# Kernel optimization log

Measured on AMD Instinct MI355X. Metric: run time of the kernel, lower is better.

## Reference

```python
import jax, jax.numpy as jnp
import numpy as np

B, S, H, NH, HD = 64, 200, 1024, 16, 64
MAX_LEN = 200
FF = 4 * H


def _ln(x, g, b):
    m = x.mean(-1, keepdims=True)
    v = ((x - m) ** 2).mean(-1, keepdims=True)
    return (x - m) / jnp.sqrt(v + 1e-5) * g + b


def setup_inputs() -> dict:
    key = jax.random.key(0)
    k = jax.random.split(key, 24)
    s = 0.02
    f32 = jnp.float32
    return {
        "x": jax.random.normal(k[0], (B, S, H), f32),
        "time": jax.random.uniform(k[1], (B, S, 1), dtype=f32),
        "wq": jax.random.normal(k[2], (H, H), f32) * s,
        "bq": jnp.zeros((H,), f32),
        "wk": jax.random.normal(k[3], (H, H), f32) * s,
        "bk": jnp.zeros((H,), f32),
        "wv": jax.random.normal(k[4], (H, H), f32) * s,
        "bv": jnp.zeros((H,), f32),
        "wo": jax.random.normal(k[5], (H, H), f32) * s,
        "bo": jnp.zeros((H,), f32),
        "wt": jax.random.normal(k[6], (1, H), f32) * s,
        "bt": jnp.zeros((H,), f32),
        "pos_embed": jax.random.normal(k[7], (2 * MAX_LEN - 1, HD), f32) * s,
        "g1": jnp.ones((H,), f32),
        "be1": jnp.zeros((H,), f32),
        "g2": jnp.ones((H,), f32),
        "be2": jnp.zeros((H,), f32),
        "w1": jax.random.normal(k[8], (H, FF), f32) * s,
        "bf1": jnp.zeros((FF,), f32),
        "w2": jax.random.normal(k[9], (FF, H), f32) * s,
        "bf2": jnp.zeros((H,), f32),
    }


def reference(x, time, wq, bq, wk, bk, wv, bv, wo, bo, wt, bt, pos_embed,
              g1, be1, g2, be2, w1, bf1, w2, bf2):
    b, s, hs = x.shape
    residual = x
    h = _ln(x, g1, be1)
    h = h + time @ wt + bt  # time embedding added post-LN
    q = (h @ wq + bq).reshape(b, s, NH, HD).transpose(0, 2, 1, 3)  # [b,h,s,d]
    k = (h @ wk + bk).reshape(b, s, NH, HD).transpose(0, 2, 1, 3)
    v = (h @ wv + bv).reshape(b, s, NH, HD).transpose(0, 2, 1, 3)
    scale = np.float32(1.0 / np.sqrt(HD))
    scores = jnp.einsum('bhqd,bhkd->bhqk', q, k) * scale
    # gathered relative position bias (NOT scaled, added after scaling)
    idx = jnp.arange(s)
    rel = jnp.clip(idx[:, None] - idx[None, :] + (MAX_LEN - 1), 0, 2 * MAX_LEN - 2)
    rel_emb = pos_embed[rel]  # [s, s, HD]
    scores = scores + jnp.einsum('bhqd,qkd->bhqk', q, rel_emb)
    causal_mask = jnp.triu(jnp.ones((s, s), bool), 1)
    scores = jnp.where(causal_mask, jnp.float32(-1e9), scores)
    attn = jax.nn.softmax(scores, axis=-1)
    ctx = jnp.einsum('bhqk,bhkd->bhqd', attn, v)
    ctx = ctx.transpose(0, 2, 1, 3).reshape(b, s, hs)
    out = ctx @ wo + bo + residual
    res2 = out
    h2 = _ln(out, g2, be2)
    ff = jax.nn.gelu(h2 @ w1 + bf1, approximate=False) @ w2 + bf2
    return ff + res2
```

## Files before the change

kernel.cpp:

```cpp
#include <hip/hip_runtime.h>

#define B_SZ   64
#define S_LEN  200
#define H_DIM  1024
#define NHEAD  16
#define HDIM   64
#define FF_DIM 4096
#define NROWS  (B_SZ * S_LEN)

typedef __bf16 bf16x8 __attribute__((ext_vector_type(8)));
typedef float  f32x4  __attribute__((ext_vector_type(4)));

#define GLOBAL_AS __attribute__((address_space(1)))
#define LDS_AS    __attribute__((address_space(3)))

__device__ __forceinline__ void g2lds16(const void* g, void* l) {
  __builtin_amdgcn_global_load_lds((const GLOBAL_AS void*)g, (LDS_AS void*)l, 16, 0, 0);
}

__device__ __forceinline__ float b2f(ushort u) {
  return __uint_as_float(((unsigned int)u) << 16);
}
__device__ __forceinline__ ushort f2b(float f) {
  unsigned int u = __float_as_uint(f);
  u += 0x7fffu + ((u >> 16) & 1u);
  return (ushort)(u >> 16);
}
__device__ __forceinline__ bf16x8 ld_g16(const ushort* p) {
  union { uint4 u; bf16x8 v; } r; r.u = *(const uint4*)p; return r.v;
}
__device__ __forceinline__ bf16x8 ld_lds8x2(const ushort* p) {
  union { uint2 u[2]; bf16x8 v; } r;
  r.u[0] = *(const uint2*)p;
  r.u[1] = *(const uint2*)(p + 4);
  return r.v;
}

__global__ __launch_bounds__(256) void transpose_to_bf16(
    const float* __restrict__ w, ushort* __restrict__ wt, int K, int N) {
  __shared__ float tile[32][33];
  int nb = blockIdx.x * 32, kb = blockIdx.y * 32;
  int tx = threadIdx.x, ty = threadIdx.y;
#pragma unroll
  for (int i = 0; i < 4; ++i) {
    int k = kb + ty + i * 8;
    tile[ty + i * 8][tx] = w[(size_t)k * N + nb + tx];
  }
  __syncthreads();
#pragma unroll
  for (int i = 0; i < 4; ++i) {
    int n = nb + ty + i * 8;
    wt[(size_t)n * K + kb + tx] = f2b(tile[tx][ty + i * 8]);
  }
}

__global__ void concat_bias(const float* __restrict__ bq, const float* __restrict__ bk,
                            const float* __restrict__ bv, float* __restrict__ o) {
  int i = blockIdx.x * 256 + threadIdx.x;
  if (i < 1024) o[i] = bq[i];
  else if (i < 2048) o[i] = bk[i - 1024];
  else if (i < 3072) o[i] = bv[i - 2048];
}

__global__ void pos_to_bf16(const float* __restrict__ pos, ushort* __restrict__ pb) {
  int i = blockIdx.x * 256 + threadIdx.x;
  pb[i] = f2b(pos[(size_t)199 * 64 + i]);
}

template <int HAS_TIME>
__global__ __launch_bounds__(256) void ln_kernel(
    const float* __restrict__ x, const float* __restrict__ g, const float* __restrict__ be,
    const float* __restrict__ tv, const float* __restrict__ wt, const float* __restrict__ bt,
    ushort* __restrict__ out) {
  int r = blockIdx.x, t = threadIdx.x;
  const float4* xr = (const float4*)(x + (size_t)r * H_DIM);
  float4 xv = xr[t];
  float s  = xv.x + xv.y + xv.z + xv.w;
  float s2 = xv.x * xv.x + xv.y * xv.y + xv.z * xv.z + xv.w * xv.w;
#pragma unroll
  for (int off = 32; off; off >>= 1) {
    s  += __shfl_xor(s, off);
    s2 += __shfl_xor(s2, off);
  }
  __shared__ float red[8];
  int lane = t & 63, wid = t >> 6;
  if (lane == 0) { red[wid] = s; red[4 + wid] = s2; }
  __syncthreads();
  float S  = red[0] + red[1] + red[2] + red[3];
  float S2 = red[4] + red[5] + red[6] + red[7];
  float m    = S * (1.0f / H_DIM);
  float var  = S2 * (1.0f / H_DIM) - m * m;
  float rstd = rsqrtf(var + 1e-5f);
  float tval = HAS_TIME ? tv[r] : 0.0f;
  float4 gv = ((const float4*)g)[t];
  float4 bv = ((const float4*)be)[t];
  float v0 = (xv.x - m) * rstd * gv.x + bv.x;
  float v1 = (xv.y - m) * rstd * gv.y + bv.y;
  float v2 = (xv.z - m) * rstd * gv.z + bv.z;
  float v3 = (xv.w - m) * rstd * gv.w + bv.w;
  if (HAS_TIME) {
    float4 wv = ((const float4*)wt)[t];
    float4 btv = ((const float4*)bt)[t];
    v0 += tval * wv.x + btv.x;
    v1 += tval * wv.y + btv.y;
    v2 += tval * wv.z + btv.z;
    v3 += tval * wv.w + btv.w;
  }
  ushort4 o;
  o.x = f2b(v0); o.y = f2b(v1); o.z = f2b(v2); o.w = f2b(v3);
  ((ushort4*)(out + (size_t)r * H_DIM))[t] = o;
}

template <int EPI>
__global__ __launch_bounds__(256) void gemm_bt(
    const ushort* __restrict__ A, const ushort* __restrict__ Bt,
    const float* __restrict__ bias, void* __restrict__ Cv,
    const float* __restrict__ resid, int M, int N, int K) {
  __shared__ __align__(16) ushort As[2 * 128 * 32];
  __shared__ __align__(16) ushort Bs[2 * 128 * 32];
  int t = threadIdx.x;
  int lane = t & 63, wave = t >> 6;
  int wm = wave >> 1, wn = wave & 1;
  int r15 = lane & 15, quad = lane >> 4;
  int nwg = gridDim.x * gridDim.y;
  int bid = blockIdx.y * gridDim.x + blockIdx.x;
  int swz = (bid & 7) * (nwg >> 3) + (bid >> 3);
  int bx = swz % gridDim.x, by = swz / gridDim.x;
  size_t row0 = (size_t)by * 128;
  size_t col0 = (size_t)bx * 128;

  int srow = (lane >> 2), scol = (lane & 3) * 8;
  const ushort* ga0 = A  + (row0 + wave * 32 +      srow) * K + scol;
  const ushort* ga1 = A  + (row0 + wave * 32 + 16 + srow) * K + scol;
  const ushort* gb0 = Bt + (col0 + wave * 32 +      srow) * K + scol;
  const ushort* gb1 = Bt + (col0 + wave * 32 + 16 + srow) * K + scol;
  ushort* la0 = As + (wave * 32) * 32;
  ushort* la1 = As + (wave * 32 + 16) * 32;
  ushort* lb0 = Bs + (wave * 32) * 32;
  ushort* lb1 = Bs + (wave * 32 + 16) * 32;

  f32x4 acc[4][4] = {};

  for (int k0 = 0; k0 < K; k0 += 64) {
#pragma unroll
    for (int kh = 0; kh < 2; ++kh) {
      int go = k0 + kh * 32, lo = kh * 4096;
      g2lds16(ga0 + go, la0 + lo);
      g2lds16(ga1 + go, la1 + lo);
      g2lds16(gb0 + go, lb0 + lo);
      g2lds16(gb1 + go, lb1 + lo);
    }
    __syncthreads();
#pragma unroll
    for (int kh = 0; kh < 2; ++kh) {
      bf16x8 af[4], bfr[4];
#pragma unroll
      for (int i = 0; i < 4; ++i)
        af[i] = *(const bf16x8*)&As[kh * 4096 + (wm * 64 + i * 16 + r15) * 32 + quad * 8];
#pragma unroll
      for (int j = 0; j < 4; ++j)
        bfr[j] = *(const bf16x8*)&Bs[kh * 4096 + (wn * 64 + j * 16 + r15) * 32 + quad * 8];
#pragma unroll
      for (int i = 0; i < 4; ++i)
#pragma unroll
        for (int j = 0; j < 4; ++j)
          acc[i][j] = __builtin_amdgcn_mfma_f32_16x16x32_bf16(af[i], bfr[j], acc[i][j], 0, 0, 0);
    }
    __syncthreads();
  }

  int mbase = (int)row0 + wm * 64;
  int nbase = (int)col0 + wn * 64;
#pragma unroll
  for (int i = 0; i < 4; ++i) {
#pragma unroll
    for (int j = 0; j < 4; ++j) {
      int col = nbase + j * 16 + r15;
      float bb = bias[col];
#pragma unroll
      for (int ii = 0; ii < 4; ++ii) {
        int row = mbase + i * 16 + quad * 4 + ii;
        size_t idx = (size_t)row * N + col;
        float v = acc[i][j][ii] + bb;
        if constexpr (EPI == 0) {
          ((ushort*)Cv)[idx] = f2b(v);
        } else if constexpr (EPI == 1) {
          float gl = 0.5f * v * (1.0f + erff(v * 0.70710678118f));
          ((ushort*)Cv)[idx] = f2b(gl);
        } else {
          ((float*)Cv)[idx] = v + resid[idx];
        }
      }
    }
  }
}

template <int IB>
__device__ __forceinline__ void mfma_blk(f32x4 (&acc)[8][4],
                                         const bf16x8 (&af)[4], const bf16x8 (&bfr)[4]) {
#pragma unroll
  for (int i = 0; i < 4; ++i)
#pragma unroll
    for (int j = 0; j < 4; ++j)
      acc[IB + i][j] =
          __builtin_amdgcn_mfma_f32_16x16x32_bf16(af[i], bfr[j], acc[IB + i][j], 0, 0, 0);
}

__device__ __forceinline__ bf16x8 rdfrag(const ushort* plane, int r, int quad) {
  return *(const bf16x8*)(plane + r * 32 + ((quad ^ ((r >> 1) & 3)) << 3));
}

__device__ __forceinline__ void read_q0(bf16x8 (&af)[4], bf16x8 (&bfr)[4],
                                        const ushort* pA, const ushort* pB,
                                        int wn1, int r15, int quad) {
#pragma unroll
  for (int j = 0; j < 4; ++j) bfr[j] = rdfrag(pB, wn1 * 64 + j * 16 + r15, quad);
#pragma unroll
  for (int i = 0; i < 4; ++i) af[i] = rdfrag(pA, i * 16 + r15, quad);
}
__device__ __forceinline__ void read_q1(bf16x8 (&af)[4], const ushort* pA,
                                        int r15, int quad) {
#pragma unroll
  for (int i = 0; i < 4; ++i) af[i] = rdfrag(pA, 64 + i * 16 + r15, quad);
}

#define VMW8() asm volatile("s_waitcnt vmcnt(8)" ::: "memory")
#define VMW4() asm volatile("s_waitcnt vmcnt(4)" ::: "memory")
#define VMW0() asm volatile("s_waitcnt vmcnt(0)" ::: "memory")
#define BARX() __builtin_amdgcn_s_barrier()
#define PRIO1() __builtin_amdgcn_s_setprio(1)
#define PRIO0() __builtin_amdgcn_s_setprio(0)

template <int EPI>
__global__ __launch_bounds__(512) void gemm256(
    const ushort* __restrict__ A, const ushort* __restrict__ Bt,
    const float* __restrict__ bias, void* __restrict__ Cv,
    const float* __restrict__ resid, int M, int N, int K) {
  __shared__ __align__(16) ushort lds[2][2][2][2][4096];
  const int t = threadIdx.x;
  const int lane = t & 63, wave = t >> 6;
  const int wm = wave >> 2;
  const int wn = wave & 3;
  const int wn1 = wn & 1;
  const int bh = wn >> 1;
  const int r15 = lane & 15, quad = lane >> 4;
  int nwg = gridDim.x * gridDim.y;
  int bid = blockIdx.y * gridDim.x + blockIdx.x;
  int swz = (bid & 7) * (nwg >> 3) + (bid >> 3);
  int bx = swz % gridDim.x, by = swz / gridDim.x;
  const size_t row0 = (size_t)by * 256;
  const size_t col0 = (size_t)bx * 256;

  const int gwA = wave & 3;
  const int gwB = ((wave >> 1) & 2) | (wave & 1);

  const ushort *gA0, *gA1, *gB0, *gB1;
  {
    int p0 = gwA * 128 + lane;
    int p1 = p0 + 64;
    int ra0 = p0 >> 2, sa0 = (p0 & 3) ^ ((p0 >> 3) & 3);
    int ra1 = p1 >> 2, sa1 = (p1 & 3) ^ ((p1 >> 3) & 3);
    gA0 = A + (row0 + wm * 128 + ra0) * K + sa0 * 8;
    gA1 = A + (row0 + wm * 128 + ra1) * K + sa1 * 8;
    int q0 = gwB * 128 + lane;
    int q1 = q0 + 64;
    int rb0 = q0 >> 2, sb0 = (q0 & 3) ^ ((q0 >> 3) & 3);
    int rb1 = q1 >> 2, sb1 = (q1 & 3) ^ ((q1 >> 3) & 3);
    gB0 = Bt + (col0 + bh * 128 + rb0) * K + sb0 * 8;
    gB1 = Bt + (col0 + bh * 128 + rb1) * K + sb1 * 8;
  }
  const int ldsA0 = gwA * 1024, ldsA1 = gwA * 1024 + 512;
  const int ldsB0 = gwB * 1024, ldsB1 = gwB * 1024 + 512;

#define STAGE_A(nb_, skh_, kof_)                                        \
  do {                                                                  \
    g2lds16(gA0 + (kof_) + (skh_) * 32, &lds[nb_][0][wm][skh_][ldsA0]); \
    g2lds16(gA1 + (kof_) + (skh_) * 32, &lds[nb_][0][wm][skh_][ldsA1]); \
  } while (0)
#define STAGE_B(nb_, skh_, kof_)                                        \
  do {                                                                  \
    g2lds16(gB0 + (kof_) + (skh_) * 32, &lds[nb_][1][bh][skh_][ldsB0]); \
    g2lds16(gB1 + (kof_) + (skh_) * 32, &lds[nb_][1][bh][skh_][ldsB1]); \
  } while (0)
#define PAP(b_, k_) (&lds[b_][0][wm][k_][0])
#define PBP(b_, k_) (&lds[b_][1][bh][k_][0])

  f32x4 acc[8][4] = {};

  STAGE_A(0, 0, 0);
  STAGE_B(0, 0, 0);
  STAGE_A(0, 1, 0);
  STAGE_B(0, 1, 0);
  STAGE_A(1, 0, 64);
  STAGE_B(1, 0, 64);
  VMW8();
  BARX();

#define ITER_BODY(LAST_, ka_)                                                  \
  {                                                                            \
    bf16x8 af[4], bfr[4];                                                      \
                                                          \
    read_q0(af, bfr, PAP(0, 0), PBP(0, 0), wn1, r15, quad);                    \
    STAGE_A(1, 1, (ka_) + 64);                                                 \
    BARX(); PRIO1(); mfma_blk<0>(acc, af, bfr); PRIO0(); BARX();               \
                                                          \
    read_q1(af, PAP(0, 0), r15, quad);                                         \
    STAGE_B(1, 1, (ka_) + 64);                                                 \
    BARX(); PRIO1(); mfma_blk<4>(acc, af, bfr); PRIO0();                       \
    VMW8(); BARX();                                                            \
                                                          \
    read_q0(af, bfr, PAP(0, 1), PBP(0, 1), wn1, r15, quad);                    \
    if (!(LAST_)) STAGE_A(0, 0, (ka_) + 128);                                  \
    BARX(); PRIO1(); mfma_blk<0>(acc, af, bfr); PRIO0(); BARX();               \
                                                          \
    read_q1(af, PAP(0, 1), r15, quad);                                         \
    if (!(LAST_)) STAGE_B(0, 0, (ka_) + 128);                                  \
    BARX(); PRIO1(); mfma_blk<4>(acc, af, bfr); PRIO0();                       \
    if (LAST_) { VMW4(); } else { VMW8(); }                                    \
    BARX();                                                                    \
                                                          \
    read_q0(af, bfr, PAP(1, 0), PBP(1, 0), wn1, r15, quad);                    \
    if (!(LAST_)) STAGE_A(0, 1, (ka_) + 128);                                  \
    BARX(); PRIO1(); mfma_blk<0>(acc, af, bfr); PRIO0(); BARX();               \
                                                          \
    read_q1(af, PAP(1, 0), r15, quad);                                         \
    if (!(LAST_)) STAGE_B(0, 1, (ka_) + 128);                                  \
    BARX(); PRIO1(); mfma_blk<4>(acc, af, bfr); PRIO0();                       \
    if (LAST_) { VMW0(); } else { VMW8(); }                                    \
    BARX();                                                                    \
                                                          \
    read_q0(af, bfr, PAP(1, 1), PBP(1, 1), wn1, r15, quad);                    \
    if (!(LAST_)) STAGE_A(1, 0, (ka_) + 192);                                  \
    BARX(); PRIO1(); mfma_blk<0>(acc, af, bfr); PRIO0(); BARX();               \
                                                          \
    read_q1(af, PAP(1, 1), r15, quad);                                         \
    if (!(LAST_)) STAGE_B(1, 0, (ka_) + 192);                                  \
    BARX(); PRIO1(); mfma_blk<4>(acc, af, bfr); PRIO0();                       \
    if (!(LAST_)) { VMW8(); }                                                  \
    BARX();                                                                    \
  }

  const int NI = K >> 7;
  for (int it = 0; it < NI - 1; ++it) {
    ITER_BODY(0, it << 7);
  }
  ITER_BODY(1, (NI - 1) << 7);
#undef ITER_BODY

  int mbase = (int)row0 + wm * 128;
  int nbase = (int)col0 + wn * 64;
#pragma unroll
  for (int j = 0; j < 4; ++j) {
    int col = nbase + j * 16 + r15;
    float bb = bias[col];
#pragma unroll
    for (int i = 0; i < 8; ++i) {
#pragma unroll
      for (int ii = 0; ii < 4; ++ii) {
        int row = mbase + i * 16 + quad * 4 + ii;
        size_t idx = (size_t)row * N + col;
        float v = acc[i][j][ii] + bb;
        if constexpr (EPI == 0) {
          ((ushort*)Cv)[idx] = f2b(v);
        } else if constexpr (EPI == 1) {
          float gl = 0.5f * v * (1.0f + erff(v * 0.70710678118f));
          ((ushort*)Cv)[idx] = f2b(gl);
        } else {
          ((float*)Cv)[idx] = v + resid[idx];
        }
      }
    }
  }
#undef STAGE_A
#undef STAGE_B
#undef PAP
#undef PBP
}

#define PW_STRIDE 228
__global__ __launch_bounds__(256) void attn_kernel(
    const ushort* __restrict__ qkv, const ushort* __restrict__ pos_bf,
    ushort* __restrict__ ctx) {
  int bh = blockIdx.x;
  int b = bh >> 4, h = bh & 15;
  __shared__ ushort Vt[64][PW_STRIDE];
  __shared__ ushort Pw[4][16][PW_STRIDE];
  int t = threadIdx.x, lane = t & 63, wave = t >> 6;
  int r15 = lane & 15, quad = lane >> 4;
  const size_t base = ((size_t)b * S_LEN) * 3072 + (size_t)h * 64;

  for (int i = t; i < 64 * 28; i += 256) Vt[i / 28][200 + (i % 28)] = 0;
  for (int i = t; i < 800; i += 256) {
    int kp = i >> 3, d0 = (i & 7) * 8;
    int k = kp * 2;
    union { uint4 v; ushort u[8]; } r0, r1;
    r0.v = *(const uint4*)&qkv[base + (size_t)k * 3072 + 2048 + d0];
    r1.v = *(const uint4*)&qkv[base + (size_t)(k + 1) * 3072 + 2048 + d0];
#pragma unroll
    for (int j = 0; j < 8; ++j) {
      ushort2 w2; w2.x = r0.u[j]; w2.y = r1.u[j];
      *(ushort2*)&Vt[d0 + j][k] = w2;
    }
  }
  __syncthreads();

  for (int qt = wave; qt < 13; qt += 4) {
    int q0 = qt * 16;
    int qrow = q0 + r15; if (qrow > 199) qrow = 199;
    const ushort* qp = qkv + base + (size_t)qrow * 3072;
    bf16x8 aq0 = ld_g16(qp + quad * 8);
    bf16x8 aq1 = ld_g16(qp + 32 + quad * 8);
    ushort* pw = &Pw[wave][0][0];

#pragma unroll
    for (int dt = 0; dt < 13; ++dt) {
      if (dt > qt) continue;
      int prow = dt * 16 + r15; if (prow > 199) prow = 199;
      const ushort* pp = pos_bf + (size_t)prow * 64;
      bf16x8 p0 = ld_g16(pp + quad * 8);
      bf16x8 p1 = ld_g16(pp + 32 + quad * 8);
      f32x4 tt = {};
      tt = __builtin_amdgcn_mfma_f32_16x16x32_bf16(aq0, p0, tt, 0, 0, 0);
      tt = __builtin_amdgcn_mfma_f32_16x16x32_bf16(aq1, p1, tt, 0, 0, 0);
#pragma unroll
      for (int ii = 0; ii < 4; ++ii)
        pw[(quad * 4 + ii) * PW_STRIDE + dt * 16 + r15] = f2b(tt[ii]);
    }

    f32x4 sreg[13];
    float rowmax[4] = {-3.0e38f, -3.0e38f, -3.0e38f, -3.0e38f};
#pragma unroll
    for (int kt = 0; kt < 13; ++kt) {
      if (kt > qt) continue;
      int krow = kt * 16 + r15; if (krow > 199) krow = 199;
      const ushort* kp = qkv + base + (size_t)krow * 3072 + 1024;
      bf16x8 k0 = ld_g16(kp + quad * 8);
      bf16x8 k1 = ld_g16(kp + 32 + quad * 8);
      f32x4 s = {};
      s = __builtin_amdgcn_mfma_f32_16x16x32_bf16(aq0, k0, s, 0, 0, 0);
      s = __builtin_amdgcn_mfma_f32_16x16x32_bf16(aq1, k1, s, 0, 0, 0);
      int k = kt * 16 + r15;
#pragma unroll
      for (int ii = 0; ii < 4; ++ii) {
        int q = q0 + quad * 4 + ii;
        float v;
        if (k <= q) {
          v = s[ii] * 0.125f + b2f(pw[(quad * 4 + ii) * PW_STRIDE + (q - k)]);
        } else {
          v = -1.0e30f;
        }
        s[ii] = v;
        rowmax[ii] = fmaxf(rowmax[ii], v);
      }
      sreg[kt] = s;
    }
#pragma unroll
    for (int off = 8; off; off >>= 1)
#pragma unroll
      for (int ii = 0; ii < 4; ++ii)
        rowmax[ii] = fmaxf(rowmax[ii], __shfl_xor(rowmax[ii], off));

    float rsum[4] = {0.f, 0.f, 0.f, 0.f};
#pragma unroll
    for (int kt = 0; kt < 13; ++kt) {
      if (kt > qt) continue;
#pragma unroll
      for (int ii = 0; ii < 4; ++ii) {
        float e = __expf(sreg[kt][ii] - rowmax[ii]);
        rsum[ii] += e;
        pw[(quad * 4 + ii) * PW_STRIDE + kt * 16 + r15] = f2b(e);
      }
    }
    if ((qt & 1) == 0) {
#pragma unroll
      for (int ii = 0; ii < 4; ++ii)
        pw[(quad * 4 + ii) * PW_STRIDE + (qt + 1) * 16 + r15] = 0;
    }
#pragma unroll
    for (int off = 8; off; off >>= 1)
#pragma unroll
      for (int ii = 0; ii < 4; ++ii)
        rsum[ii] += __shfl_xor(rsum[ii], off);
    float rinv[4];
#pragma unroll
    for (int ii = 0; ii < 4; ++ii) rinv[ii] = 1.0f / rsum[ii];

    int nk = (q0 + 15) / 32 + 1;
    f32x4 acc[4] = {};
#pragma unroll
    for (int k32 = 0; k32 < 7; ++k32) {
      if (k32 >= nk) continue;
      bf16x8 ap = ld_lds8x2(&pw[r15 * PW_STRIDE + k32 * 32 + quad * 8]);
#pragma unroll
      for (int n = 0; n < 4; ++n) {
        bf16x8 bv = ld_lds8x2(&Vt[n * 16 + r15][k32 * 32 + quad * 8]);
        acc[n] = __builtin_amdgcn_mfma_f32_16x16x32_bf16(ap, bv, acc[n], 0, 0, 0);
      }
    }
#pragma unroll
    for (int n = 0; n < 4; ++n)
#pragma unroll
      for (int ii = 0; ii < 4; ++ii) {
        int q = q0 + quad * 4 + ii;
        if (q < S_LEN)
          ctx[((size_t)(b * S_LEN + q)) * H_DIM + h * 64 + n * 16 + r15] =
              f2b(acc[n][ii] * rinv[ii]);
      }
  }
}

extern "C" void kernel_launch(void* const* d_in, const int* in_sizes, int n_in,
                              void* d_out, int out_size, void* d_ws, size_t ws_size,
                              hipStream_t stream) {
  (void)in_sizes; (void)n_in; (void)out_size; (void)ws_size;
  const float* x    = (const float*)d_in[0];
  const float* timev= (const float*)d_in[1];
  const float* wq   = (const float*)d_in[2];
  const float* bq   = (const float*)d_in[3];
  const float* wk   = (const float*)d_in[4];
  const float* bk   = (const float*)d_in[5];
  const float* wv   = (const float*)d_in[6];
  const float* bv   = (const float*)d_in[7];
  const float* wo   = (const float*)d_in[8];
  const float* bo   = (const float*)d_in[9];
  const float* wt   = (const float*)d_in[10];
  const float* bt   = (const float*)d_in[11];
  const float* pos  = (const float*)d_in[12];
  const float* g1   = (const float*)d_in[13];
  const float* be1  = (const float*)d_in[14];
  const float* g2   = (const float*)d_in[15];
  const float* be2  = (const float*)d_in[16];
  const float* w1   = (const float*)d_in[17];
  const float* bf1  = (const float*)d_in[18];
  const float* w2   = (const float*)d_in[19];
  const float* bf2  = (const float*)d_in[20];

  char* ws = (char*)d_ws;
  ushort* wqkv_t = (ushort*)ws;   ws += (size_t)3072 * 1024 * 2;
  ushort* wo_t   = (ushort*)ws;   ws += (size_t)1024 * 1024 * 2;
  ushort* w1_t   = (ushort*)ws;   ws += (size_t)4096 * 1024 * 2;
  ushort* w2_t   = (ushort*)ws;   ws += (size_t)1024 * 4096 * 2;
  float*  bqkv   = (float*)ws;    ws += (size_t)16384;
  ushort* pos_bf = (ushort*)ws;   ws += (size_t)200 * 64 * 2;
  char* r1 = ws;                  ws += (size_t)NROWS * 3072 * 2;
  ushort* qkv  = (ushort*)r1;
  ushort* h2   = (ushort*)r1;
  ushort* gbuf = (ushort*)(r1 + (size_t)NROWS * H_DIM * 2);
  char* r2 = ws;                  ws += (size_t)NROWS * 1024 * 2;
  ushort* hbf = (ushort*)r2;
  ushort* ctx = (ushort*)r2;
  float* res2 = (float*)d_out;

  dim3 tb(32, 8);
  transpose_to_bf16<<<dim3(32, 32), tb, 0, stream>>>(wq, wqkv_t,                 1024, 1024);
  transpose_to_bf16<<<dim3(32, 32), tb, 0, stream>>>(wk, wqkv_t + 1024 * 1024,   1024, 1024);
  transpose_to_bf16<<<dim3(32, 32), tb, 0, stream>>>(wv, wqkv_t + 2048 * 1024,   1024, 1024);
  transpose_to_bf16<<<dim3(32, 32), tb, 0, stream>>>(wo, wo_t,                   1024, 1024);
  transpose_to_bf16<<<dim3(128, 32), tb, 0, stream>>>(w1, w1_t,                  1024, 4096);
  transpose_to_bf16<<<dim3(32, 128), tb, 0, stream>>>(w2, w2_t,                  4096, 1024);
  concat_bias<<<12, 256, 0, stream>>>(bq, bk, bv, bqkv);
  pos_to_bf16<<<50, 256, 0, stream>>>(pos, pos_bf);

  ln_kernel<1><<<NROWS, 256, 0, stream>>>(x, g1, be1, timev, wt, bt, hbf);

  gemm256<0><<<dim3(12, 50), 512, 0, stream>>>(hbf, wqkv_t, bqkv, qkv, nullptr,
                                               NROWS, 3072, 1024);
  attn_kernel<<<B_SZ * NHEAD, 256, 0, stream>>>(qkv, pos_bf, ctx);

  gemm256<2><<<dim3(4, 50), 512, 0, stream>>>(ctx, wo_t, bo, res2, x,
                                              NROWS, 1024, 1024);
  ln_kernel<0><<<NROWS, 256, 0, stream>>>(res2, g2, be2, nullptr, nullptr, nullptr, h2);

  for (int c = 0; c < 2; ++c) {
    size_t ro = (size_t)c * 6400;
    gemm256<1><<<dim3(16, 25), 512, 0, stream>>>(h2 + ro * 1024, w1_t, bf1, gbuf, nullptr,
                                                 6400, 4096, 1024);
    gemm_bt<2><<<dim3(8, 50), 256, 0, stream>>>(gbuf, w2_t, bf2, (float*)d_out + ro * 1024,
                                                res2 + ro * 1024, 6400, 1024, 4096);
  }
}
```

Measured before the change: 802.0 us.

## Merge prep kernels, use wave-per-row LayerNorm, reorder tile swizzle and attention tiles

Replaces the eight weight-transpose, bias-concat and pos-conversion launches with a single prep kernel. LayerNorm now handles one row per wave, which removes the LDS reduction and block barrier. GEMM tile swizzle now maps consecutive swizzled ids along M rather than N. GEMM epilogues hoist the bias loads and iterate rows before columns. Attention waves take query tiles in a permuted order to balance causal work. Together these cut launch overhead and sync cost but change cache reuse patterns for the GEMMs.

```diff
diff --git a/kernel.cpp b/kernel.cpp
--- a/kernel.cpp
+++ b/kernel.cpp
@@ -36,35 +36,47 @@
   return r.v;
 }
 
-__global__ __launch_bounds__(256) void transpose_to_bf16(
-    const float* __restrict__ w, ushort* __restrict__ wt, int K, int N) {
-  __shared__ float tile[32][33];
-  int nb = blockIdx.x * 32, kb = blockIdx.y * 32;
-  int tx = threadIdx.x, ty = threadIdx.y;
-#pragma unroll
-  for (int i = 0; i < 4; ++i) {
-    int k = kb + ty + i * 8;
-    tile[ty + i * 8][tx] = w[(size_t)k * N + nb + tx];
-  }
-  __syncthreads();
-#pragma unroll
-  for (int i = 0; i < 4; ++i) {
-    int n = nb + ty + i * 8;
-    wt[(size_t)n * K + kb + tx] = f2b(tile[tx][ty + i * 8]);
-  }
-}
-
-__global__ void concat_bias(const float* __restrict__ bq, const float* __restrict__ bk,
-                            const float* __restrict__ bv, float* __restrict__ o) {
-  int i = blockIdx.x * 256 + threadIdx.x;
-  if (i < 1024) o[i] = bq[i];
-  else if (i < 2048) o[i] = bk[i - 1024];
-  else if (i < 3072) o[i] = bv[i - 2048];
-}
-
-__global__ void pos_to_bf16(const float* __restrict__ pos, ushort* __restrict__ pb) {
-  int i = blockIdx.x * 256 + threadIdx.x;
-  pb[i] = f2b(pos[(size_t)199 * 64 + i]);
+__global__ __launch_bounds__(256) void prep_kernel(
+    const float* __restrict__ wq, const float* __restrict__ wk,
+    const float* __restrict__ wv, const float* __restrict__ wo,
+    const float* __restrict__ w1, const float* __restrict__ w2,
+    const float* __restrict__ bq, const float* __restrict__ bk,
+    const float* __restrict__ bv_, const float* __restrict__ pos,
+    ushort* __restrict__ wqkv_t, ushort* __restrict__ wo_t,
+    ushort* __restrict__ w1_t, ushort* __restrict__ w2_t,
+    float* __restrict__ bqkv, ushort* __restrict__ pos_bf) {
+  int id = blockIdx.x;
+  if (id < 12288) {
+    const float* src; ushort* dst; int K, N, tile;
+    if (id < 4096) {
+      K = 1024; N = 1024; tile = id & 1023;
+      int m = id >> 10;
+      src = (m == 0) ? wq : (m == 1) ? wk : (m == 2) ? wv : wo;
+      dst = (m == 3) ? wo_t : wqkv_t + (size_t)m * 1024 * 1024;
+    } else if (id < 8192) {
+      K = 1024; N = 4096; tile = id - 4096; src = w1; dst = w1_t;
+    } else {
+      K = 4096; N = 1024; tile = id - 8192; src = w2; dst = w2_t;
+    }
+    int nx = N >> 5;
+    int nb = (tile % nx) * 32, kb = (tile / nx) * 32;
+    __shared__ float t32[32][33];
+    int tx = threadIdx.x & 31, ty = threadIdx.x >> 5;
+#pragma unroll
+    for (int i = 0; i < 4; ++i)
+      t32[ty + i * 8][tx] = src[(size_t)(kb + ty + i * 8) * N + nb + tx];
+    __syncthreads();
+#pragma unroll
+    for (int i = 0; i < 4; ++i)
+      dst[(size_t)(nb + ty + i * 8) * K + kb + tx] = f2b(t32[tx][ty + i * 8]);
+  } else {
+    int t = threadIdx.x;
+    for (int i = t; i < 1024; i += 256) {
+      bqkv[i] = bq[i]; bqkv[1024 + i] = bk[i]; bqkv[2048 + i] = bv_[i];
+    }
+    for (int i = t; i < 12800; i += 256)
+      pos_bf[i] = f2b(pos[(size_t)199 * 64 + i]);
+  }
 }
 
 template <int HAS_TIME>
@@ -72,43 +84,47 @@
     const float* __restrict__ x, const float* __restrict__ g, const float* __restrict__ be,
     const float* __restrict__ tv, const float* __restrict__ wt, const float* __restrict__ bt,
     ushort* __restrict__ out) {
-  int r = blockIdx.x, t = threadIdx.x;
+  int wave = threadIdx.x >> 6, lane = threadIdx.x & 63;
+  int r = blockIdx.x * 4 + wave;
   const float4* xr = (const float4*)(x + (size_t)r * H_DIM);
-  float4 xv = xr[t];
-  float s  = xv.x + xv.y + xv.z + xv.w;
-  float s2 = xv.x * xv.x + xv.y * xv.y + xv.z * xv.z + xv.w * xv.w;
+  float4 xv[4];
+  float s = 0.f, s2 = 0.f;
+#pragma unroll
+  for (int k = 0; k < 4; ++k) {
+    xv[k] = xr[lane + 64 * k];
+    s  += xv[k].x + xv[k].y + xv[k].z + xv[k].w;
+    s2 += xv[k].x * xv[k].x + xv[k].y * xv[k].y + xv[k].z * xv[k].z + xv[k].w * xv[k].w;
+  }
 #pragma unroll
   for (int off = 32; off; off >>= 1) {
     s  += __shfl_xor(s, off);
     s2 += __shfl_xor(s2, off);
   }
-  __shared__ float red[8];
-  int lane = t & 63, wid = t >> 6;
-  if (lane == 0) { red[wid] = s; red[4 + wid] = s2; }
-  __syncthreads();
-  float S  = red[0] + red[1] + red[2] + red[3];
-  float S2 = red[4] + red[5] + red[6] + red[7];
-  float m    = S * (1.0f / H_DIM);
-  float var  = S2 * (1.0f / H_DIM) - m * m;
+  float m    = s * (1.0f / H_DIM);
+  float var  = s2 * (1.0f / H_DIM) - m * m;
   float rstd = rsqrtf(var + 1e-5f);
   float tval = HAS_TIME ? tv[r] : 0.0f;
-  float4 gv = ((const float4*)g)[t];
-  float4 bv = ((const float4*)be)[t];
-  float v0 = (xv.x - m) * rstd * gv.x + bv.x;
-  float v1 = (xv.y - m) * rstd * gv.y + bv.y;
-  float v2 = (xv.z - m) * rstd * gv.z + bv.z;
-  float v3 = (xv.w - m) * rstd * gv.w + bv.w;
-  if (HAS_TIME) {
-    float4 wv = ((const float4*)wt)[t];
-    float4 btv = ((const float4*)bt)[t];
-    v0 += tval * wv.x + btv.x;
-    v1 += tval * wv.y + btv.y;
-    v2 += tval * wv.z + btv.z;
-    v3 += tval * wv.w + btv.w;
-  }
-  ushort4 o;
-  o.x = f2b(v0); o.y = f2b(v1); o.z = f2b(v2); o.w = f2b(v3);
-  ((ushort4*)(out + (size_t)r * H_DIM))[t] = o;
+  ushort4* orow = (ushort4*)(out + (size_t)r * H_DIM);
+#pragma unroll
+  for (int k = 0; k < 4; ++k) {
+    float4 gv = ((const float4*)g)[lane + 64 * k];
+    float4 bv = ((const float4*)be)[lane + 64 * k];
+    float v0 = (xv[k].x - m) * rstd * gv.x + bv.x;
+    float v1 = (xv[k].y - m) * rstd * gv.y + bv.y;
+    float v2 = (xv[k].z - m) * rstd * gv.z + bv.z;
+    float v3 = (xv[k].w - m) * rstd * gv.w + bv.w;
+    if (HAS_TIME) {
+      float4 wv = ((const float4*)wt)[lane + 64 * k];
+      float4 btv = ((const float4*)bt)[lane + 64 * k];
+      v0 += tval * wv.x + btv.x;
+      v1 += tval * wv.y + btv.y;
+      v2 += tval * wv.z + btv.z;
+      v3 += tval * wv.w + btv.w;
+    }
+    ushort4 o;
+    o.x = f2b(v0); o.y = f2b(v1); o.z = f2b(v2); o.w = f2b(v3);
+    orow[lane + 64 * k] = o;
+  }
 }
 
 template <int EPI>
@@ -125,7 +141,7 @@
   int nwg = gridDim.x * gridDim.y;
   int bid = blockIdx.y * gridDim.x + blockIdx.x;
   int swz = (bid & 7) * (nwg >> 3) + (bid >> 3);
-  int bx = swz % gridDim.x, by = swz / gridDim.x;
+  int by = swz % gridDim.y, bx = swz / gridDim.y;
   size_t row0 = (size_t)by * 128;
   size_t col0 = (size_t)bx * 128;
 
@@ -171,17 +187,19 @@
 
   int mbase = (int)row0 + wm * 64;
   int nbase = (int)col0 + wn * 64;
+  float bb[4];
+#pragma unroll
+  for (int j = 0; j < 4; ++j) bb[j] = bias[nbase + j * 16 + r15];
 #pragma unroll
   for (int i = 0; i < 4; ++i) {
 #pragma unroll
-    for (int j = 0; j < 4; ++j) {
-      int col = nbase + j * 16 + r15;
-      float bb = bias[col];
-#pragma unroll
-      for (int ii = 0; ii < 4; ++ii) {
-        int row = mbase + i * 16 + quad * 4 + ii;
-        size_t idx = (size_t)row * N + col;
-        float v = acc[i][j][ii] + bb;
+    for (int ii = 0; ii < 4; ++ii) {
+      int row = mbase + i * 16 + quad * 4 + ii;
+      size_t rb = (size_t)row * N + nbase + r15;
+#pragma unroll
+      for (int j = 0; j < 4; ++j) {
+        size_t idx = rb + j * 16;
+        float v = acc[i][j][ii] + bb[j];
         if constexpr (EPI == 0) {
           ((ushort*)Cv)[idx] = f2b(v);
         } else if constexpr (EPI == 1) {
@@ -247,7 +265,7 @@
   int nwg = gridDim.x * gridDim.y;
   int bid = blockIdx.y * gridDim.x + blockIdx.x;
   int swz = (bid & 7) * (nwg >> 3) + (bid >> 3);
-  int bx = swz % gridDim.x, by = swz / gridDim.x;
+  int by = swz % gridDim.y, bx = swz / gridDim.y;
   const size_t row0 = (size_t)by * 256;
   const size_t col0 = (size_t)bx * 256;
 
@@ -349,17 +367,19 @@
 
   int mbase = (int)row0 + wm * 128;
   int nbase = (int)col0 + wn * 64;
-#pragma unroll
-  for (int j = 0; j < 4; ++j) {
-    int col = nbase + j * 16 + r15;
-    float bb = bias[col];
-#pragma unroll
-    for (int i = 0; i < 8; ++i) {
-#pragma unroll
-      for (int ii = 0; ii < 4; ++ii) {
-        int row = mbase + i * 16 + quad * 4 + ii;
-        size_t idx = (size_t)row * N + col;
-        float v = acc[i][j][ii] + bb;
+  float bb[4];
+#pragma unroll
+  for (int j = 0; j < 4; ++j) bb[j] = bias[nbase + j * 16 + r15];
+#pragma unroll
+  for (int i = 0; i < 8; ++i) {
+#pragma unroll
+    for (int ii = 0; ii < 4; ++ii) {
+      int row = mbase + i * 16 + quad * 4 + ii;
+      size_t rb = (size_t)row * N + nbase + r15;
+#pragma unroll
+      for (int j = 0; j < 4; ++j) {
+        size_t idx = rb + j * 16;
+        float v = acc[i][j][ii] + bb[j];
         if constexpr (EPI == 0) {
           ((ushort*)Cv)[idx] = f2b(v);
         } else if constexpr (EPI == 1) {
@@ -404,7 +424,8 @@
   }
   __syncthreads();
 
-  for (int qt = wave; qt < 13; qt += 4) {
+  for (int idx = wave; idx < 13; idx += 4) {
+    int qt = (int)((0x3421058769ABCull >> (4 * idx)) & 0xFull);
     int q0 = qt * 16;
     int qrow = q0 + r15; if (qrow > 199) qrow = 199;
     const ushort* qp = qkv + base + (size_t)qrow * 3072;
@@ -551,17 +572,10 @@
   ushort* ctx = (ushort*)r2;
   float* res2 = (float*)d_out;
 
-  dim3 tb(32, 8);
-  transpose_to_bf16<<<dim3(32, 32), tb, 0, stream>>>(wq, wqkv_t,                 1024, 1024);
-  transpose_to_bf16<<<dim3(32, 32), tb, 0, stream>>>(wk, wqkv_t + 1024 * 1024,   1024, 1024);
-  transpose_to_bf16<<<dim3(32, 32), tb, 0, stream>>>(wv, wqkv_t + 2048 * 1024,   1024, 1024);
-  transpose_to_bf16<<<dim3(32, 32), tb, 0, stream>>>(wo, wo_t,                   1024, 1024);
-  transpose_to_bf16<<<dim3(128, 32), tb, 0, stream>>>(w1, w1_t,                  1024, 4096);
-  transpose_to_bf16<<<dim3(32, 128), tb, 0, stream>>>(w2, w2_t,                  4096, 1024);
-  concat_bias<<<12, 256, 0, stream>>>(bq, bk, bv, bqkv);
-  pos_to_bf16<<<50, 256, 0, stream>>>(pos, pos_bf);
-
-  ln_kernel<1><<<NROWS, 256, 0, stream>>>(x, g1, be1, timev, wt, bt, hbf);
+  prep_kernel<<<12289, 256, 0, stream>>>(wq, wk, wv, wo, w1, w2, bq, bk, bv, pos,
+                                         wqkv_t, wo_t, w1_t, w2_t, bqkv, pos_bf);
+
+  ln_kernel<1><<<NROWS / 4, 256, 0, stream>>>(x, g1, be1, timev, wt, bt, hbf);
 
   gemm256<0><<<dim3(12, 50), 512, 0, stream>>>(hbf, wqkv_t, bqkv, qkv, nullptr,
                                                NROWS, 3072, 1024);
@@ -569,7 +583,7 @@
 
   gemm256<2><<<dim3(4, 50), 512, 0, stream>>>(ctx, wo_t, bo, res2, x,
                                               NROWS, 1024, 1024);
-  ln_kernel<0><<<NROWS, 256, 0, stream>>>(res2, g2, be2, nullptr, nullptr, nullptr, h2);
+  ln_kernel<0><<<NROWS / 4, 256, 0, stream>>>(res2, g2, be2, nullptr, nullptr, nullptr, h2);
 
   for (int c = 0; c < 2; ++c) {
     size_t ro = (size_t)c * 6400;
```

New measurement: 773.9 us. 1.04x faster.
